# Kernel tuning notes

Hardware: AMD Instinct MI355X
Metric: run time of the kernel (lower is better)

The kernel has to match this reference:

```python
import jax, jax.numpy as jnp
import numpy as np

D_MODEL = 2048
NUM_HEADS = 16
HEAD_DIM = D_MODEL // NUM_HEADS
SEQ_LEN = 2048
NEG_BIG = -1000000000.0


def setup_inputs() -> dict:
    key = jax.random.key(0)
    ks = jax.random.split(key, 9)
    x = jax.random.normal(ks[0], (SEQ_LEN, D_MODEL), dtype=jnp.float32)
    # causal mask: 1.0 where attention is disallowed (strictly upper triangular)
    mask = jnp.triu(jnp.ones((SEQ_LEN, SEQ_LEN), dtype=jnp.float32), k=1)
    s = 1.0 / np.sqrt(D_MODEL)  # eqx.nn.Linear default init scale ~ U(-1/sqrt(in), 1/sqrt(in))
    def lin(kw, kb):
        W = jax.random.uniform(kw, (D_MODEL, D_MODEL), jnp.float32, -s, s)
        b = jax.random.uniform(kb, (D_MODEL,), jnp.float32, -s, s)
        return W, b
    Wq, bq = lin(ks[1], ks[2])
    Wk, bk = lin(ks[3], ks[4])
    Wv, bv = lin(ks[5], ks[6])
    Wo, bo = lin(ks[7], ks[8])
    return {"x": x, "mask": mask, "Wq": Wq, "bq": bq, "Wk": Wk, "bk": bk,
            "Wv": Wv, "bv": bv, "Wo": Wo, "bo": bo}


def reference(x, mask, Wq, bq, Wk, bk, Wv, bv, Wo, bo):
    seq_len = x.shape[0]
    # eqx.nn.Linear computes W @ x + b per token -> x @ W.T + b for a batch of tokens
    Q = (x @ Wq.T + bq).reshape(seq_len, NUM_HEADS, HEAD_DIM)
    K = (x @ Wk.T + bk).reshape(seq_len, NUM_HEADS, HEAD_DIM)
    V = (x @ Wv.T + bv).reshape(seq_len, NUM_HEADS, HEAD_DIM)
    # (h, s, s) scores
    scores = jnp.einsum("qhd,khd->hqk", Q, K) / jnp.sqrt(jnp.float32(HEAD_DIM))
    scores = scores + mask * NEG_BIG  # mask broadcasts over heads
    weights = jax.nn.softmax(scores, axis=-1)
    attn = jnp.einsum("hqk,khd->qhd", weights, V).reshape(seq_len, D_MODEL)
    return attn @ Wo.T + bo
```

## Files before the change

kernel.cpp:

```cpp
#include <hip/hip_runtime.h>

typedef __attribute__((ext_vector_type(8))) short bf16x8;
typedef __attribute__((ext_vector_type(4))) float f32x4;

#define MFMA16(a, b, c) __builtin_amdgcn_mfma_f32_16x16x32_bf16(a, b, c, 0, 0, 0)

typedef __attribute__((address_space(3))) void lds_t;
typedef __attribute__((address_space(1))) const void gbl_t;
#define ASYNC_COPY16(g, l) __builtin_amdgcn_global_load_lds((gbl_t*)(g), (lds_t*)(l), 16, 0, 0)

constexpr int DM  = 2048;
constexpr int SQL = 2048;
constexpr int NH  = 16;
constexpr int HD  = 128;
constexpr int HSZ = SQL * HD;
constexpr size_t NW = (size_t)DM * DM;
constexpr size_t NB = DM;

__device__ __forceinline__ float b2f(short s) {
    union { unsigned u; float f; } v;
    v.u = ((unsigned)(unsigned short)s) << 16;
    return v.f;
}
__device__ __forceinline__ short f2b(float f) {
    union { float f; unsigned u; } v; v.f = f;
    unsigned r = 0x7fffu + ((v.u >> 16) & 1u);
    return (short)((v.u + r) >> 16);
}

__global__ __launch_bounds__(256) void convert_inputs(
    const void* x, const void* wq, const void* bq, const void* wk, const void* bk,
    const void* wv, const void* bv, const void* wo, const void* bo,
    const unsigned* __restrict__ maskw, short* __restrict__ dst)
{
    const size_t offs[10] = {0, NW, 2*NW, 2*NW+NB, 3*NW+NB, 3*NW+2*NB,
                             4*NW+2*NB, 4*NW+3*NB, 5*NW+3*NB, 5*NW+4*NB};
    const void* srcs[9] = {x, wq, bq, wk, bk, wv, bv, wo, bo};
    size_t i8 = (size_t)(blockIdx.x * 256 + threadIdx.x) * 8;
    if (i8 >= offs[9]) return;
    int seg = 0;
    while (i8 >= offs[seg + 1]) ++seg;
    const size_t loc = i8 - offs[seg];
    if (maskw[0] == 0u) {
        const float* s = (const float*)srcs[seg] + loc;
        const float4 a = *(const float4*)s;
        const float4 c = *(const float4*)(s + 4);
        short t[8];
        t[0] = f2b(a.x); t[1] = f2b(a.y); t[2] = f2b(a.z); t[3] = f2b(a.w);
        t[4] = f2b(c.x); t[5] = f2b(c.y); t[6] = f2b(c.z); t[7] = f2b(c.w);
        *(ushort4*)(dst + i8)     = *(ushort4*)t;
        *(ushort4*)(dst + i8 + 4) = *(ushort4*)(t + 4);
    } else {
        *(int4*)(dst + i8) = *(const int4*)((const short*)srcs[seg] + loc);
    }
}

__global__ __launch_bounds__(256) void gemm_nt(
    const short* __restrict__ A,
    const short* B0, const short* bias0, void* C0,
    const short* B1, const short* bias1, void* C1,
    const short* B2, const short* bias2, void* C2,
    int mode)
{
    __shared__ __align__(16) short As[128 * 64];
    __shared__ __align__(16) short Bs[128 * 64];

    const int z = blockIdx.z;
    const short* B; const short* bias; void* C; int kbeg, kend;
    if (mode == 1) {
        B = B0; bias = bias0; C = (z == 0) ? C0 : C1;
        kbeg = z * 1024; kend = kbeg + 1024;
    } else {
        B    = (z == 0) ? B0    : ((z == 1) ? B1    : B2);
        bias = (z == 0) ? bias0 : ((z == 1) ? bias1 : bias2);
        C    = (z == 0) ? C0    : ((z == 1) ? C1    : C2);
        kbeg = 0; kend = DM;
    }

    const int m0 = blockIdx.y * 128;
    const int n0 = blockIdx.x * 128;
    const int t    = threadIdx.x;
    const int lane = t & 63;
    const int wv   = t >> 6;
    const int rw = (wv >> 1) * 64;
    const int cw = (wv & 1) * 64;
    const int r16  = lane & 15;
    const int quad = lane >> 4;
    const int pr   = r16 & 7;

    const int sr8 = lane >> 3;
    const int sch = (lane & 7) ^ sr8;
    const short* gA0 = A + (size_t)(m0 + wv * 32 + sr8) * DM + sch * 8;
    const short* gB0 = B + (size_t)(n0 + wv * 32 + sr8) * DM + sch * 8;
    short* lA = As + (wv * 32) * 64;
    short* lB = Bs + (wv * 32) * 64;

    f32x4 zero = {0.f, 0.f, 0.f, 0.f};
    f32x4 acc[4][4];
    #pragma unroll
    for (int i = 0; i < 4; ++i)
        #pragma unroll
        for (int j = 0; j < 4; ++j) acc[i][j] = zero;

    for (int k0 = kbeg; k0 < kend; k0 += 64) {
        __syncthreads();
        #pragma unroll
        for (int c = 0; c < 4; ++c) {
            ASYNC_COPY16(gA0 + (size_t)(c * 8) * DM + k0, lA + c * 512);
            ASYNC_COPY16(gB0 + (size_t)(c * 8) * DM + k0, lB + c * 512);
        }
        __syncthreads();

        #pragma unroll
        for (int ks = 0; ks < 2; ++ks) {
            bf16x8 af[4], bfr[4];
            #pragma unroll
            for (int i = 0; i < 4; ++i)
                af[i] = *(const bf16x8*)(As + (rw + i * 16 + r16) * 64
                                         + (((ks * 4 + quad) ^ pr) << 3));
            #pragma unroll
            for (int j = 0; j < 4; ++j)
                bfr[j] = *(const bf16x8*)(Bs + (cw + j * 16 + r16) * 64
                                          + (((ks * 4 + quad) ^ pr) << 3));
            #pragma unroll
            for (int i = 0; i < 4; ++i)
                #pragma unroll
                for (int j = 0; j < 4; ++j)
                    acc[i][j] = MFMA16(af[i], bfr[j], acc[i][j]);
        }
    }

    if (mode == 1) {
        float* Cf = (float*)C;
        #pragma unroll
        for (int j = 0; j < 4; ++j) {
            const int col = n0 + cw + j * 16 + r16;
            #pragma unroll
            for (int i = 0; i < 4; ++i) {
                const int rbase = m0 + rw + i * 16 + quad * 4;
                #pragma unroll
                for (int r = 0; r < 4; ++r)
                    Cf[(size_t)(rbase + r) * DM + col] = acc[i][j][r];
            }
        }
    } else if (z == 1) {
        short* Cs = (short*)C;
        #pragma unroll
        for (int j = 0; j < 4; ++j) {
            const int col = n0 + cw + j * 16 + r16;
            const float bj = b2f(bias[col]);
            const int head = col >> 7, chunk = (col & 127) >> 3, wi = col & 7;
            #pragma unroll
            for (int i = 0; i < 4; ++i) {
                const int rbase = m0 + rw + i * 16 + quad * 4;
                #pragma unroll
                for (int r = 0; r < 4; ++r) {
                    const int seq = rbase + r;
                    Cs[(size_t)head * HSZ + seq * 128 + ((chunk ^ (seq & 15)) << 3) + wi]
                        = f2b(acc[i][j][r] + bj);
                }
            }
        }
    } else if (z == 2) {
        short* Cs = (short*)C;
        #pragma unroll
        for (int j = 0; j < 4; ++j) {
            const int col = n0 + cw + j * 16 + r16;
            const float bj = b2f(bias[col]);
            const int head = col >> 7, dimh = col & 127;
            #pragma unroll
            for (int i = 0; i < 4; ++i) {
                const int rbase = m0 + rw + i * 16 + quad * 4;
                const int kb = rbase >> 6, key0 = rbase & 63;
                const int pos = (key0 >> 3) ^ (dimh & 7);
                ushort4 pk;
                pk.x = (unsigned short)f2b(acc[i][j][0] + bj);
                pk.y = (unsigned short)f2b(acc[i][j][1] + bj);
                pk.z = (unsigned short)f2b(acc[i][j][2] + bj);
                pk.w = (unsigned short)f2b(acc[i][j][3] + bj);
                *(ushort4*)(Cs + (size_t)head * HSZ + kb * 8192 + dimh * 64
                            + pos * 8 + (key0 & 7)) = pk;
            }
        }
    } else {
        short* Cs = (short*)C;
        #pragma unroll
        for (int j = 0; j < 4; ++j) {
            const int col = n0 + cw + j * 16 + r16;
            const float bj = b2f(bias[col]);
            #pragma unroll
            for (int i = 0; i < 4; ++i) {
                const int rbase = m0 + rw + i * 16 + quad * 4;
                #pragma unroll
                for (int r = 0; r < 4; ++r)
                    Cs[(size_t)(rbase + r) * DM + col] = f2b(acc[i][j][r] + bj);
            }
        }
    }
}

__global__ __launch_bounds__(256) void finalize_out(
    const float* __restrict__ P0, const float* __restrict__ P1,
    const short* __restrict__ bias, void* __restrict__ out,
    const unsigned* __restrict__ maskw)
{
    const size_t i4 = (size_t)(blockIdx.x * 256 + threadIdx.x) * 4;
    const float4 a = *(const float4*)(P0 + i4);
    const float4 b = *(const float4*)(P1 + i4);
    const int col = (int)(i4 & 2047);
    const float s0 = a.x + b.x + b2f(bias[col]);
    const float s1 = a.y + b.y + b2f(bias[col + 1]);
    const float s2 = a.z + b.z + b2f(bias[col + 2]);
    const float s3 = a.w + b.w + b2f(bias[col + 3]);
    if (maskw[0] == 0u) {
        float4 o = {s0, s1, s2, s3};
        *(float4*)((float*)out + i4) = o;
    } else {
        ushort4 o;
        o.x = (unsigned short)f2b(s0); o.y = (unsigned short)f2b(s1);
        o.z = (unsigned short)f2b(s2); o.w = (unsigned short)f2b(s3);
        *(ushort4*)((short*)out + i4) = o;
    }
}

__global__ __launch_bounds__(256, 4) void attn_fwd(
    const short* __restrict__ Q, const short* __restrict__ K2,
    const short* __restrict__ V2, short* __restrict__ O)
{
    __shared__ __align__(16) short Ks[64 * 128];
    __shared__ __align__(16) short Vs[128 * 64];
    __shared__ __align__(16) char  Ub[8192];

    short* PsA = (short*)Ub;
    short* PsB = (short*)Ub + 1024;
    float* Lr  = (float*)Ub;

    const int h = blockIdx.y;
    const int t    = threadIdx.x;
    const int lane = t & 63;
    const int wv   = t >> 6;
    const int r16  = lane & 15;
    const int quad = lane >> 4;
    const int pr   = r16 & 7;
    const float CC = 0.12751785f;

    const int i    = (blockIdx.x + 13 * blockIdx.y) & 63;
    const int q0A  = (127 - i) * 16;
    const int q0B  = i * 16;
    const int nkbA = (q0A >> 6) + 1;
    const int nkbB = (q0B >> 6) + 1;

    bf16x8 aqA[4], aqB[4];
    {
        const short* qa = Q + (size_t)(q0A + r16) * DM + h * HD + quad * 8;
        const short* qb = Q + (size_t)(q0B + r16) * DM + h * HD + quad * 8;
        #pragma unroll
        for (int s = 0; s < 4; ++s) {
            aqA[s] = *(const bf16x8*)(qa + s * 32);
            aqB[s] = *(const bf16x8*)(qb + s * 32);
        }
    }

    f32x4 zero = {0.f, 0.f, 0.f, 0.f};
    f32x4 oaccA[2] = {zero, zero}, oaccB[2] = {zero, zero};
    f32x4 lpvA = zero, lpvB = zero;

    const short* kh = K2 + (size_t)h * HSZ;
    const short* vh = V2 + (size_t)h * HSZ;
    const int pchunk = wv * 2 + (r16 >> 3);

    for (int kb = 0; kb < nkbA; ++kb) {
        const bool doB = (kb < nkbB);

        __syncthreads();
        const short* gK = kh + (size_t)kb * 8192;
        const short* gV = vh + (size_t)kb * 8192;
        #pragma unroll
        for (int c = 0; c < 4; ++c) {
            const int off = (wv * 4 + c) * 512;
            ASYNC_COPY16(gK + off + lane * 8, Ks + off);
            ASYNC_COPY16(gV + off + lane * 8, Vs + off);
        }
        __syncthreads();

        f32x4 scA = zero, scB = zero;
        const int krow = wv * 16 + r16;
        if (doB) {
            #pragma unroll
            for (int s = 0; s < 4; ++s) {
                const bf16x8 kf = *(const bf16x8*)(Ks + krow * 128 + (((s * 4 + quad) ^ r16) << 3));
                scA = MFMA16(aqA[s], kf, scA);
                scB = MFMA16(aqB[s], kf, scB);
            }
        } else {
            #pragma unroll
            for (int s = 0; s < 4; ++s) {
                const bf16x8 kf = *(const bf16x8*)(Ks + krow * 128 + (((s * 4 + quad) ^ r16) << 3));
                scA = MFMA16(aqA[s], kf, scA);
            }
        }

        const int colk = kb * 64 + wv * 16 + r16;
        {
            const bool dA = (kb == nkbA - 1);
            #pragma unroll
            for (int r = 0; r < 4; ++r) {
                const int row = quad * 4 + r;
                float e = __builtin_amdgcn_exp2f(scA[r] * CC);
                if (dA && colk > q0A + row) e = 0.f;
                lpvA[r] += e;
                PsA[row * 64 + ((pchunk ^ (row & 7)) << 3) + (r16 & 7)] = f2b(e);
            }
        }
        if (doB) {
            const bool dB = (kb == nkbB - 1);
            #pragma unroll
            for (int r = 0; r < 4; ++r) {
                const int row = quad * 4 + r;
                float e = __builtin_amdgcn_exp2f(scB[r] * CC);
                if (dB && colk > q0B + row) e = 0.f;
                lpvB[r] += e;
                PsB[row * 64 + ((pchunk ^ (row & 7)) << 3) + (r16 & 7)] = f2b(e);
            }
        }
        __syncthreads();

        const bf16x8 apA0 = *(const bf16x8*)(PsA + r16 * 64 + ((quad ^ pr) << 3));
        const bf16x8 apA1 = *(const bf16x8*)(PsA + r16 * 64 + (((4 + quad) ^ pr) << 3));
        if (doB) {
            const bf16x8 apB0 = *(const bf16x8*)(PsB + r16 * 64 + ((quad ^ pr) << 3));
            const bf16x8 apB1 = *(const bf16x8*)(PsB + r16 * 64 + (((4 + quad) ^ pr) << 3));
            #pragma unroll
            for (int nt = 0; nt < 2; ++nt) {
                const int dim = wv * 32 + nt * 16 + r16;
                const bf16x8 v0 = *(const bf16x8*)(Vs + dim * 64 + ((quad ^ pr) << 3));
                const bf16x8 v1 = *(const bf16x8*)(Vs + dim * 64 + (((4 + quad) ^ pr) << 3));
                oaccA[nt] = MFMA16(apA0, v0, oaccA[nt]);
                oaccA[nt] = MFMA16(apA1, v1, oaccA[nt]);
                oaccB[nt] = MFMA16(apB0, v0, oaccB[nt]);
                oaccB[nt] = MFMA16(apB1, v1, oaccB[nt]);
            }
        } else {
            #pragma unroll
            for (int nt = 0; nt < 2; ++nt) {
                const int dim = wv * 32 + nt * 16 + r16;
                const bf16x8 v0 = *(const bf16x8*)(Vs + dim * 64 + ((quad ^ pr) << 3));
                const bf16x8 v1 = *(const bf16x8*)(Vs + dim * 64 + (((4 + quad) ^ pr) << 3));
                oaccA[nt] = MFMA16(apA0, v0, oaccA[nt]);
                oaccA[nt] = MFMA16(apA1, v1, oaccA[nt]);
            }
        }
    }

    __syncthreads();
    *(f32x4*)(Lr + (wv * 64 + lane) * 4)       = lpvA;
    *(f32x4*)(Lr + ((4 + wv) * 64 + lane) * 4) = lpvB;
    __syncthreads();
    f32x4 lsA = zero, lsB = zero;
    #pragma unroll
    for (int w = 0; w < 4; ++w) {
        lsA += *(const f32x4*)(Lr + (w * 64 + lane) * 4);
        lsB += *(const f32x4*)(Lr + ((4 + w) * 64 + lane) * 4);
    }
    float invA[4], invB[4];
    #pragma unroll
    for (int r = 0; r < 4; ++r) {
        float la = lsA[r], lb = lsB[r];
        #pragma unroll
        for (int d = 1; d < 16; d <<= 1) {
            la += __shfl_xor(la, d);
            lb += __shfl_xor(lb, d);
        }
        invA[r] = 1.f / la;
        invB[r] = 1.f / lb;
    }
    #pragma unroll
    for (int nt = 0; nt < 2; ++nt) {
        const int col = h * HD + wv * 32 + nt * 16 + r16;
        #pragma unroll
        for (int r = 0; r < 4; ++r) {
            O[(size_t)(q0A + quad * 4 + r) * DM + col] = f2b(oaccA[nt][r] * invA[r]);
            O[(size_t)(q0B + quad * 4 + r) * DM + col] = f2b(oaccB[nt][r] * invB[r]);
        }
    }
}

extern "C" void kernel_launch(void* const* d_in, const int* in_sizes, int n_in,
                              void* d_out, int out_size, void* d_ws, size_t ws_size,
                              hipStream_t stream) {
    const unsigned* maskw = (const unsigned*)d_in[1];

    short* canon = (short*)d_ws;
    const short* X  = canon;
    const short* WQ = canon + NW;
    const short* BQ = canon + 2*NW;
    const short* WK = canon + 2*NW + NB;
    const short* BK = canon + 3*NW + NB;
    const short* WV = canon + 3*NW + 2*NB;
    const short* BV = canon + 4*NW + 2*NB;
    const short* WO = canon + 4*NW + 3*NB;
    const short* BO = canon + 5*NW + 3*NB;
    short* Qb = canon + 5*NW + 4*NB;
    short* K2 = Qb + NW;
    short* V2 = K2 + NW;
    short* At = V2 + NW;
    float* Pp0 = (float*)canon;
    float* Pp1 = (float*)(canon + 2*NW + NB);

    const size_t total8 = (5*NW + 4*NB) / 8;
    convert_inputs<<<dim3((unsigned)((total8 + 255) / 256)), dim3(256), 0, stream>>>(
        d_in[0], d_in[2], d_in[3], d_in[4], d_in[5], d_in[6], d_in[7], d_in[8], d_in[9],
        maskw, canon);

    gemm_nt<<<dim3(16, 16, 3), dim3(256), 0, stream>>>(
        X, WQ, BQ, Qb, WK, BK, K2, WV, BV, V2, 0);

    attn_fwd<<<dim3(64, NH), dim3(256), 0, stream>>>(Qb, K2, V2, At);

    gemm_nt<<<dim3(16, 16, 2), dim3(256), 0, stream>>>(
        At, WO, BO, Pp0, WO, BO, Pp1, WO, BO, Pp1, 1);
    finalize_out<<<dim3(4096), dim3(256), 0, stream>>>(Pp0, Pp1, BO, d_out, maskw);
}
```

Measured before the change: 308.5 us.

## Replace 256-thread GEMM with single-wave double-buffered 64x64 tile kernel

Rewrites the projection GEMM as one-wavefront blocks computing 64x64 tiles with K steps of 32. Async global-to-LDS copies are double-buffered and ordered with vmcnt waits instead of block barriers. The aim is to remove __syncthreads stalls and overlap loads with MFMA. In exchange each tile reuses data less, so more global and L2 traffic is needed, and the grid grows to 1024 blocks per z-slice.

After: 358.6 us. 16.2% more time.

```diff
diff --git a/kernel.cpp b/kernel.cpp
--- a/kernel.cpp
+++ b/kernel.cpp
@@ -8,6 +8,8 @@
 typedef __attribute__((address_space(3))) void lds_t;
 typedef __attribute__((address_space(1))) const void gbl_t;
 #define ASYNC_COPY16(g, l) __builtin_amdgcn_global_load_lds((gbl_t*)(g), (lds_t*)(l), 16, 0, 0)
+#define WAIT_VM8() __builtin_amdgcn_s_waitcnt(0xF78)
+#define WAIT_VM0() __builtin_amdgcn_s_waitcnt(0xF70)
 
 constexpr int DM  = 2048;
 constexpr int SQL = 2048;
@@ -55,45 +57,39 @@
     }
 }
 
-__global__ __launch_bounds__(256) void gemm_nt(
+__global__ __launch_bounds__(64) void gemm_wp(
     const short* __restrict__ A,
     const short* B0, const short* bias0, void* C0,
     const short* B1, const short* bias1, void* C1,
     const short* B2, const short* bias2, void* C2,
     int mode)
 {
-    __shared__ __align__(16) short As[128 * 64];
-    __shared__ __align__(16) short Bs[128 * 64];
-
-    const int z = blockIdx.z;
-    const short* B; const short* bias; void* C; int kbeg, kend;
+    __shared__ __align__(16) short Ab[2][64 * 32];
+    __shared__ __align__(16) short Bb[2][64 * 32];
+
+    const int z = blockIdx.y;
+    const short* B; const short* bias; void* C; int kbeg, niter;
     if (mode == 1) {
         B = B0; bias = bias0; C = (z == 0) ? C0 : C1;
-        kbeg = z * 1024; kend = kbeg + 1024;
+        kbeg = z * 1024; niter = 1024 / 32;
     } else {
         B    = (z == 0) ? B0    : ((z == 1) ? B1    : B2);
         bias = (z == 0) ? bias0 : ((z == 1) ? bias1 : bias2);
         C    = (z == 0) ? C0    : ((z == 1) ? C1    : C2);
-        kbeg = 0; kend = DM;
-    }
-
-    const int m0 = blockIdx.y * 128;
-    const int n0 = blockIdx.x * 128;
-    const int t    = threadIdx.x;
-    const int lane = t & 63;
-    const int wv   = t >> 6;
-    const int rw = (wv >> 1) * 64;
-    const int cw = (wv & 1) * 64;
+        kbeg = 0; niter = DM / 32;
+    }
+
+    const int bx = blockIdx.x;
+    const int m0 = (bx >> 5) * 64;
+    const int n0 = (bx & 31) * 64;
+    const int lane = threadIdx.x;
     const int r16  = lane & 15;
     const int quad = lane >> 4;
-    const int pr   = r16 & 7;
-
-    const int sr8 = lane >> 3;
-    const int sch = (lane & 7) ^ sr8;
-    const short* gA0 = A + (size_t)(m0 + wv * 32 + sr8) * DM + sch * 8;
-    const short* gB0 = B + (size_t)(n0 + wv * 32 + sr8) * DM + sch * 8;
-    short* lA = As + (wv * 32) * 64;
-    short* lB = Bs + (wv * 32) * 64;
+
+    const int srow = lane >> 2;
+    const int sch  = (lane & 3) ^ (srow & 3);
+    const short* gA = A + (size_t)(m0 + srow) * DM + sch * 8 + kbeg;
+    const short* gB = B + (size_t)(n0 + srow) * DM + sch * 8 + kbeg;
 
     f32x4 zero = {0.f, 0.f, 0.f, 0.f};
     f32x4 acc[4][4];
@@ -102,42 +98,54 @@
         #pragma unroll
         for (int j = 0; j < 4; ++j) acc[i][j] = zero;
 
-    for (int k0 = kbeg; k0 < kend; k0 += 64) {
-        __syncthreads();
-        #pragma unroll
-        for (int c = 0; c < 4; ++c) {
-            ASYNC_COPY16(gA0 + (size_t)(c * 8) * DM + k0, lA + c * 512);
-            ASYNC_COPY16(gB0 + (size_t)(c * 8) * DM + k0, lB + c * 512);
-        }
-        __syncthreads();
-
-        #pragma unroll
-        for (int ks = 0; ks < 2; ++ks) {
-            bf16x8 af[4], bfr[4];
-            #pragma unroll
-            for (int i = 0; i < 4; ++i)
-                af[i] = *(const bf16x8*)(As + (rw + i * 16 + r16) * 64
-                                         + (((ks * 4 + quad) ^ pr) << 3));
-            #pragma unroll
-            for (int j = 0; j < 4; ++j)
-                bfr[j] = *(const bf16x8*)(Bs + (cw + j * 16 + r16) * 64
-                                          + (((ks * 4 + quad) ^ pr) << 3));
-            #pragma unroll
-            for (int i = 0; i < 4; ++i)
-                #pragma unroll
-                for (int j = 0; j < 4; ++j)
-                    acc[i][j] = MFMA16(af[i], bfr[j], acc[i][j]);
-        }
-    }
+    const int foff = r16 * 32 + ((quad ^ (r16 & 3)) << 3);
+
+    #define STAGE(buf, kk)                                                     \
+        { const int koff = (kk) * 32;                                          \
+          _Pragma("unroll")                                                    \
+          for (int c = 0; c < 4; ++c) {                                        \
+              ASYNC_COPY16(gA + (size_t)(c * 16) * DM + koff, &Ab[buf][c*512]);\
+              ASYNC_COPY16(gB + (size_t)(c * 16) * DM + koff, &Bb[buf][c*512]);\
+          } }
+
+    #define CONSUME(buf)                                                       \
+        { bf16x8 af[4], bfr[4];                                                \
+          _Pragma("unroll")                                                    \
+          for (int i = 0; i < 4; ++i)                                          \
+              af[i] = *(const bf16x8*)(&Ab[buf][i * 512 + foff]);              \
+          _Pragma("unroll")                                                    \
+          for (int j = 0; j < 4; ++j)                                          \
+              bfr[j] = *(const bf16x8*)(&Bb[buf][j * 512 + foff]);             \
+          _Pragma("unroll")                                                    \
+          for (int i = 0; i < 4; ++i)                                          \
+              _Pragma("unroll")                                                \
+              for (int j = 0; j < 4; ++j)                                      \
+                  acc[i][j] = MFMA16(af[i], bfr[j], acc[i][j]); }
+
+    STAGE(0, 0);
+    for (int k = 0; k < niter; k += 2) {
+        STAGE(1, k + 1);
+        WAIT_VM8();
+        CONSUME(0);
+        if (k + 2 < niter) {
+            STAGE(0, k + 2);
+            WAIT_VM8();
+        } else {
+            WAIT_VM0();
+        }
+        CONSUME(1);
+    }
+    #undef STAGE
+    #undef CONSUME
 
     if (mode == 1) {
         float* Cf = (float*)C;
         #pragma unroll
         for (int j = 0; j < 4; ++j) {
-            const int col = n0 + cw + j * 16 + r16;
+            const int col = n0 + j * 16 + r16;
             #pragma unroll
             for (int i = 0; i < 4; ++i) {
-                const int rbase = m0 + rw + i * 16 + quad * 4;
+                const int rbase = m0 + i * 16 + quad * 4;
                 #pragma unroll
                 for (int r = 0; r < 4; ++r)
                     Cf[(size_t)(rbase + r) * DM + col] = acc[i][j][r];
@@ -147,12 +155,12 @@
         short* Cs = (short*)C;
         #pragma unroll
         for (int j = 0; j < 4; ++j) {
-            const int col = n0 + cw + j * 16 + r16;
+            const int col = n0 + j * 16 + r16;
             const float bj = b2f(bias[col]);
             const int head = col >> 7, chunk = (col & 127) >> 3, wi = col & 7;
             #pragma unroll
             for (int i = 0; i < 4; ++i) {
-                const int rbase = m0 + rw + i * 16 + quad * 4;
+                const int rbase = m0 + i * 16 + quad * 4;
                 #pragma unroll
                 for (int r = 0; r < 4; ++r) {
                     const int seq = rbase + r;
@@ -165,12 +173,12 @@
         short* Cs = (short*)C;
         #pragma unroll
         for (int j = 0; j < 4; ++j) {
-            const int col = n0 + cw + j * 16 + r16;
+            const int col = n0 + j * 16 + r16;
             const float bj = b2f(bias[col]);
             const int head = col >> 7, dimh = col & 127;
             #pragma unroll
             for (int i = 0; i < 4; ++i) {
-                const int rbase = m0 + rw + i * 16 + quad * 4;
+                const int rbase = m0 + i * 16 + quad * 4;
                 const int kb = rbase >> 6, key0 = rbase & 63;
                 const int pos = (key0 >> 3) ^ (dimh & 7);
                 ushort4 pk;
@@ -186,11 +194,11 @@
         short* Cs = (short*)C;
         #pragma unroll
         for (int j = 0; j < 4; ++j) {
-            const int col = n0 + cw + j * 16 + r16;
+            const int col = n0 + j * 16 + r16;
             const float bj = b2f(bias[col]);
             #pragma unroll
             for (int i = 0; i < 4; ++i) {
-                const int rbase = m0 + rw + i * 16 + quad * 4;
+                const int rbase = m0 + i * 16 + quad * 4;
                 #pragma unroll
                 for (int r = 0; r < 4; ++r)
                     Cs[(size_t)(rbase + r) * DM + col] = f2b(acc[i][j][r] + bj);
@@ -412,12 +420,12 @@
         d_in[0], d_in[2], d_in[3], d_in[4], d_in[5], d_in[6], d_in[7], d_in[8], d_in[9],
         maskw, canon);
 
-    gemm_nt<<<dim3(16, 16, 3), dim3(256), 0, stream>>>(
+    gemm_wp<<<dim3(1024, 3), dim3(64), 0, stream>>>(
         X, WQ, BQ, Qb, WK, BK, K2, WV, BV, V2, 0);
 
     attn_fwd<<<dim3(64, NH), dim3(256), 0, stream>>>(Qb, K2, V2, At);
 
-    gemm_nt<<<dim3(16, 16, 2), dim3(256), 0, stream>>>(
+    gemm_wp<<<dim3(1024, 2), dim3(64), 0, stream>>>(
         At, WO, BO, Pp0, WO, BO, Pp1, WO, BO, Pp1, 1);
     finalize_out<<<dim3(4096), dim3(256), 0, stream>>>(Pp0, Pp1, BO, d_out, maskw);
 }
```
